# Kernel tuning notes

Hardware: AMD Instinct MI355X
Metric: run time of the kernel (lower is better)

The kernel has to match this reference:

```python
import jax, jax.numpy as jnp
from jax import lax
import numpy as np

B, L, C, PRED = 64, 512, 321, 96
PATCH, STRIDE = 16, 8
N = (L - PATCH) // STRIDE + 1 + 1  # 64 patches (after replication pad)
HID = PATCH * 2                    # expansion_factor=2
ALPHA, EPS = 0.2, 1e-5

def gelu(v):
    return jax.nn.gelu(v, approximate=False)  # torch nn.GELU default (erf)

def setup_inputs() -> dict:
    key = jax.random.key(0)
    ks = jax.random.split(key, 10)
    init = lambda k, s: (jax.random.normal(k, s) * 0.02).astype(jnp.float32)
    return dict(
        x=jax.random.normal(ks[0], (B, L, C), jnp.float32),
        rev_w=jnp.ones((C,), jnp.float32), rev_b=jnp.zeros((C,), jnp.float32),
        fc1_w=init(ks[1], (HID, PATCH)), fc1_b=jnp.zeros((HID,), jnp.float32),
        bn1_w=jnp.ones((N,), jnp.float32), bn1_b=jnp.zeros((N,), jnp.float32),
        conv_w=init(ks[2], (N, 1, 3)), conv_b=jnp.zeros((N,), jnp.float32),
        bn2_w=jnp.ones((N,), jnp.float32), bn2_b=jnp.zeros((N,), jnp.float32),
        fc2_w=init(ks[3], (PATCH, HID)), fc2_b=jnp.zeros((PATCH,), jnp.float32),
        m1_w=init(ks[4], (2 * N, N)), m1_b=jnp.zeros((2 * N,), jnp.float32),
        m2_w=init(ks[5], (N, 2 * N)), m2_b=jnp.zeros((N,), jnp.float32),
        gl_scale=jnp.full((1,), 0.1, jnp.float32),
        ln_w=jnp.ones((PATCH,), jnp.float32), ln_b=jnp.zeros((PATCH,), jnp.float32),
        seas_w=init(ks[6], (PRED, N * PATCH)), seas_b=jnp.zeros((PRED,), jnp.float32),
        tr_w=init(ks[7], (PRED, L)), tr_b=jnp.zeros((PRED,), jnp.float32),
        fus_w=init(ks[8], (PRED, 2 * PRED)), fus_b=jnp.zeros((PRED,), jnp.float32),
    )

def _batchnorm(h, w, b):
    # BatchNorm1d over channel axis N (train-mode batch stats, biased var)
    mu = h.mean((0, 2), keepdims=True)
    var = h.var((0, 2), keepdims=True)
    return (h - mu) * lax.rsqrt(var + EPS) * w[None, :, None] + b[None, :, None]

def reference(x, rev_w, rev_b, fc1_w, fc1_b, bn1_w, bn1_b, conv_w, conv_b,
              bn2_w, bn2_b, fc2_w, fc2_b, m1_w, m1_b, m2_w, m2_b, gl_scale,
              ln_w, ln_b, seas_w, seas_b, tr_w, tr_b, fus_w, fus_b):
    # --- RevIN norm (torch std is unbiased, ddof=1) ---
    mean = x.mean(1, keepdims=True)
    std = jnp.std(x, axis=1, ddof=1, keepdims=True) + EPS
    xn = (x - mean) / std * rev_w + rev_b
    # --- EMA trend/seasonal decomposition via scan ---
    xt = jnp.moveaxis(xn, 1, 0)                      # [L,B,C]
    def step(c, xi):
        t = ALPHA * xi + (1.0 - ALPHA) * c
        return t, t
    _, rest = lax.scan(step, xt[0], xt[1:])
    trend = jnp.moveaxis(jnp.concatenate([xt[:1], rest], 0), 0, 1)  # [B,L,C]
    seasonal = xn - trend
    # --- patching (replication pad right by STRIDE, unfold) ---
    s = seasonal.transpose(0, 2, 1).reshape(B * C, L)
    s = jnp.concatenate([s, jnp.broadcast_to(s[:, -1:], (B * C, STRIDE))], axis=1)
    idx = np.arange(N)[:, None] * STRIDE + np.arange(PATCH)[None, :]
    sp = s[:, idx]                                    # [B*C, N, PATCH]
    # --- IntraPatch (local): fc1 -> GELU -> BN -> depthwise conv -> GELU -> BN -> fc2 + res ---
    h = gelu(sp @ fc1_w.T + fc1_b)                    # [BC,N,HID]
    h = _batchnorm(h, bn1_w, bn1_b)
    h = lax.conv_general_dilated(h, conv_w, (1,), ((1, 1),),
                                 feature_group_count=N,
                                 dimension_numbers=('NCH', 'OIH', 'NCH'))
    h = h + conv_b[None, :, None]
    h = _batchnorm(gelu(h), bn2_w, bn2_b)
    local = h @ fc2_w.T + fc2_b + sp                  # dropout is identity (eval)
    # --- InterPatch (global): pool -> MLP -> sigmoid gate ---
    pooled = sp.mean(-1)                              # [BC,N]
    w = jax.nn.sigmoid(gelu(pooled @ m1_w.T + m1_b) @ m2_w.T + m2_b)
    glob = sp * (1.0 + gl_scale * w[..., None])
    # --- fusion 'add' + residual LayerNorm over PATCH ---
    y = sp + local + glob
    mu = y.mean(-1, keepdims=True)
    var = y.var(-1, keepdims=True)
    y = (y - mu) * lax.rsqrt(var + EPS) * ln_w + ln_b
    # --- heads ---
    s_pred = y.reshape(B * C, N * PATCH) @ seas_w.T + seas_b
    t = trend.transpose(0, 2, 1).reshape(B * C, L)
    t_pred = t @ tr_w.T + tr_b
    out = jnp.concatenate([s_pred, t_pred], -1) @ fus_w.T + fus_b
    out = out.reshape(B, C, PRED).transpose(0, 2, 1)  # [B,PRED,C]
    # --- RevIN denorm ---
    out = (out - rev_b) / rev_w
    return out * std + mean
```

## Files before the change

### kernel.cpp

```cpp
#include <hip/hip_runtime.h>
#include <hip/hip_bf16.h>
#include <math.h>

#define B_    64
#define L_    512
#define C_    321
#define PRED_ 96
#define N_    64
#define HID_  32
#define BC_   (B_*C_)
#define SROW_ 528
#define EPS_  1e-5f
#define ALPHA_ 0.2f
#define GR_   16
#define RB_   8
#define NBLK2_ (BC_/GR_)
#define NBLKH_ (BC_/8)
#define D64_  6.2771017353866808e-7f
#define STW_  548
#define UTW_  260

typedef __attribute__((ext_vector_type(8))) short bf16x8;
typedef __attribute__((ext_vector_type(4))) float f32x4;

__device__ __forceinline__ float gelu_f(float x){
  float ax = fabsf(x);
  float z  = ax * 0.70710678118654752440f;
  float t  = __builtin_amdgcn_rcpf(fmaf(0.3275911f, z, 1.0f));
  float poly = fmaf(fmaf(fmaf(fmaf(1.061405429f, t, -1.453152027f),
                   t, 1.421413741f), t, -0.284496736f), t, 0.254829592f) * t;
  float e  = __expf(-z*z);
  float erfp = fmaf(-poly, e, 1.0f);
  return fmaf(0.5f*ax, erfp, 0.5f*x);
}
__device__ __forceinline__ unsigned short bf16bits(float x){
  __hip_bfloat16 h = __float2bfloat16(x);
  return *(unsigned short*)&h;
}
__device__ __forceinline__ bf16x8 cvt8(const float* p){
  float4 a = *(const float4*)p;
  float4 b = *(const float4*)(p+4);
  bf16x8 v;
  v[0]=(short)bf16bits(a.x); v[1]=(short)bf16bits(a.y);
  v[2]=(short)bf16bits(a.z); v[3]=(short)bf16bits(a.w);
  v[4]=(short)bf16bits(b.x); v[5]=(short)bf16bits(b.y);
  v[6]=(short)bf16bits(b.z); v[7]=(short)bf16bits(b.w);
  return v;
}

__global__ __launch_bounds__(256) void k1_all(
    const float* __restrict__ x, const float* __restrict__ rev_w, const float* __restrict__ rev_b,
    const float* __restrict__ seas_w, const float* __restrict__ tr_w, const float* __restrict__ fus_w,
    const float* __restrict__ seas_b, const float* __restrict__ tr_b, const float* __restrict__ fus_b,
    float* __restrict__ s_raw, __hip_bfloat16* __restrict__ t_bf, float* __restrict__ rowpar,
    float* __restrict__ pooled,
    __hip_bfloat16* __restrict__ Wsf, __hip_bfloat16* __restrict__ Wtf,
    float* __restrict__ biasc, float* __restrict__ colsumT) {
  __shared__ float lf[8][32];
  __shared__ float psum[8][32], psq[8][32];
  __shared__ float fs[8][32];
  __shared__ float st[32*STW_];
  int tid = threadIdx.x;
  int bid = blockIdx.x;
  if (bid >= BC_/32) {
    int fb = bid - BC_/32;
    if (fb < 576) {
      int idx = fb*256 + tid;
      int j = idx / 1536, k = idx - j*1536;
      float acc = 0.f;
      if (k < 1024) {
        for (int i=0;i<96;++i) acc = fmaf(fus_w[j*192+i], seas_w[i*1024+k], acc);
        Wsf[(size_t)j*1024 + k] = __float2bfloat16(acc);
      } else {
        int l = k - 1024;
        for (int i=0;i<96;++i) acc = fmaf(fus_w[j*192+96+i], tr_w[i*512+l], acc);
        Wtf[(size_t)j*512 + l] = __float2bfloat16(acc);
      }
    } else {
      __shared__ float rowsum[96];
      if (tid < 96) {
        float s = 0.f;
        for (int l=0;l<512;++l) s += tr_w[tid*512+l];
        rowsum[tid] = s;
      }
      __syncthreads();
      if (tid < 96) {
        float acc = fus_b[tid], cs = 0.f;
        for (int i=0;i<96;++i) {
          acc = fmaf(fus_w[tid*192+i],    seas_b[i], acc);
          acc = fmaf(fus_w[tid*192+96+i], tr_b[i],   acc);
          cs  = fmaf(fus_w[tid*192+96+i], rowsum[i], cs);
        }
        biasc[tid] = acc; colsumT[tid] = cs;
      }
    }
    return;
  }
  int q = tid >> 5, r = tid & 31;
  int row0 = bid*32;
  int row = row0 + r;
  int b = row / C_, c = row - b*C_;
  const float* xp = x + (size_t)b*L_*C_ + c;
  int l0 = q*64;
  float sreg[64];
  float loc = 0.f, sum = 0.f, sq = 0.f;
  #pragma unroll
  for (int i=0;i<64;++i) {
    float v = xp[(size_t)(l0+i)*C_];
    sum += v; sq = fmaf(v,v,sq);
    loc = (q==0 && i==0) ? v : fmaf(ALPHA_, v, 0.8f*loc);
    sreg[i] = loc;
  }
  lf[q][r] = loc; psum[q][r] = sum; psq[q][r] = sq;
  __syncthreads();
  float cin = 0.f;
  for (int j=0;j<q;++j) cin = fmaf(D64_, cin, lf[j][r]);
  float S=0.f, Q=0.f;
  #pragma unroll
  for (int qq=0;qq<8;++qq){ S += psum[qq][r]; Q += psq[qq][r]; }
  float mean = S*(1.0f/512.0f);
  float var  = (Q - S*S*(1.0f/512.0f))*(1.0f/511.0f);
  var = fmaxf(var, 0.f);
  float stdv = sqrtf(var) + EPS_;
  float rwc = rev_w[c];
  float a = rwc / stdv;
  if (q==0) {
    float rbc = rev_b[c];
    float g = rbc - mean*a;
    float inva = stdv / rwc;
    ((float4*)rowpar)[row] = make_float4(a, g, mean, inva);
  }
  float prev = 0.f, f = 1.f, slast = 0.f;
  float sums8[8];
  #pragma unroll
  for (int j=0;j<8;++j) sums8[j] = 0.f;
  #pragma unroll
  for (int i=0;i<64;++i) {
    float lc = sreg[i];
    f *= 0.8f;
    float s = (q==0 && i==0) ? 0.f : fmaf(4.f, lc - prev, -f*cin);
    prev = lc;
    float sv = s * a;
    st[r*STW_ + q*64 + i] = sv;
    sums8[i>>3] += sv;
    slast = sv;
  }
  fs[q][r] = sums8[0];
  if (q==7) {
    #pragma unroll
    for (int k=0;k<8;++k) st[r*STW_ + 512 + k] = slast;
  }
  __syncthreads();
  for (int idx=tid; idx<32*130; idx+=256) {
    int rr = idx/130, g = idx - rr*130;
    float4 v = *(float4*)&st[rr*STW_ + g*4];
    *(float4*)&s_raw[(size_t)(row0+rr)*SROW_ + g*4] = v;
  }
  {
    float nf = (q < 7) ? fs[q+1][r] : 8.0f*slast;
    #pragma unroll
    for (int j=0;j<7;++j)
      pooled[(size_t)row*64 + q*8 + j] = (sums8[j] + sums8[j+1])*(1.0f/16.0f);
    pooled[(size_t)row*64 + q*8 + 7] = (sums8[7] + nf)*(1.0f/16.0f);
  }
  __syncthreads();
  unsigned* tb = (unsigned*)st;
  {
    float f2 = 1.f; unsigned lo = 0;
    #pragma unroll
    for (int i=0;i<64;++i) {
      f2 *= 0.8f;
      float tt = fmaf(f2, cin, sreg[i]) * a;
      unsigned hb = bf16bits(tt);
      if ((i&1)==0) lo = hb;
      else tb[r*UTW_ + q*32 + (i>>1)] = lo | (hb<<16);
    }
  }
  __syncthreads();
  for (int idx=tid; idx<32*64; idx+=256) {
    int rr = idx>>6, g = idx&63;
    uint4 v = *(uint4*)&tb[rr*UTW_ + g*4];
    *(uint4*)&t_bf[(size_t)(row0+rr)*512 + g*8] = v;
  }
}

__global__ __launch_bounds__(512) void k4_gate(
    const float* __restrict__ pooled,
    const float* __restrict__ m1_w, const float* __restrict__ m1_b,
    const float* __restrict__ m2_w, const float* __restrict__ m2_b,
    float* __restrict__ wl_g) {
  __shared__ __align__(16) __hip_bfloat16 buf[17408];
  int t = threadIdx.x;
  int row0 = blockIdx.x*64;
  __hip_bfloat16* A1 = buf;
  __hip_bfloat16* B1 = buf + 4608;
  __hip_bfloat16* H1 = buf;
  __hip_bfloat16* B2 = buf + 8704;
  for (int idx=t; idx<4096; idx+=512) {
    int r = idx>>6, k = idx&63;
    A1[r*72+k] = __float2bfloat16(pooled[(size_t)(row0+r)*64 + k]);
  }
  for (int idx=t; idx<8192; idx+=512) {
    int r = idx>>6, k = idx&63;
    B1[r*72+k] = __float2bfloat16(m1_w[idx]);
  }
  __syncthreads();
  int lane = t & 63, w = t >> 6;
  int fr = lane & 15, fg = lane >> 4;
  int mt = w & 3;
  int ng0 = (w>>2)*4;
  f32x4 acc1[4];
  #pragma unroll
  for (int nn=0;nn<4;++nn) acc1[nn] = (f32x4){0.f,0.f,0.f,0.f};
  #pragma unroll
  for (int ksub=0; ksub<2; ++ksub) {
    bf16x8 av = *(bf16x8*)&A1[(mt*16+fr)*72 + ksub*32 + fg*8];
    #pragma unroll
    for (int nn=0;nn<4;++nn) {
      bf16x8 bv = *(bf16x8*)&B1[((ng0+nn)*16+fr)*72 + ksub*32 + fg*8];
      acc1[nn] = __builtin_amdgcn_mfma_f32_16x16x32_bf16(av, bv, acc1[nn], 0,0,0);
    }
  }
  __syncthreads();
  #pragma unroll
  for (int nn=0;nn<4;++nn) {
    int col = (ng0+nn)*16 + fr;
    float bias = m1_b[col];
    #pragma unroll
    for (int reg=0;reg<4;++reg) {
      int row = mt*16 + fg*4 + reg;
      H1[row*136 + col] = __float2bfloat16(gelu_f(acc1[nn][reg] + bias));
    }
  }
  for (int idx=t; idx<8192; idx+=512) {
    int r = idx>>7, k = idx&127;
    B2[r*136+k] = __float2bfloat16(m2_w[idx]);
  }
  __syncthreads();
  int nt0 = (w>>2)*2;
  f32x4 acc2[2];
  #pragma unroll
  for (int nn=0;nn<2;++nn) acc2[nn] = (f32x4){0.f,0.f,0.f,0.f};
  #pragma unroll
  for (int ksub=0; ksub<4; ++ksub) {
    bf16x8 av = *(bf16x8*)&H1[(mt*16+fr)*136 + ksub*32 + fg*8];
    #pragma unroll
    for (int nn=0;nn<2;++nn) {
      bf16x8 bv = *(bf16x8*)&B2[((nt0+nn)*16+fr)*136 + ksub*32 + fg*8];
      acc2[nn] = __builtin_amdgcn_mfma_f32_16x16x32_bf16(av, bv, acc2[nn], 0,0,0);
    }
  }
  #pragma unroll
  for (int nn=0;nn<2;++nn) {
    int col = (nt0+nn)*16 + fr;
    float bias = m2_b[col];
    #pragma unroll
    for (int reg=0;reg<4;++reg) {
      int row = mt*16 + fg*4 + reg;
      wl_g[(size_t)(row0+row)*64 + col] = 1.0f/(1.0f + __expf(-(acc2[nn][reg] + bias)));
    }
  }
}

__global__ __launch_bounds__(256) void k2_bn1stats(
    const float* __restrict__ s_raw,
    const float* __restrict__ fc1_w, const float* __restrict__ fc1_b,
    float* __restrict__ partials) {
  __shared__ float sl[GR_*SROW_];
  __shared__ float red[2][GR_*64];
  int t = threadIdx.x;
  int row0 = blockIdx.x*GR_;
  for (int idx=t; idx<GR_*520; idx+=256) {
    int rr = idx/520, cc = idx - rr*520;
    sl[rr*SROW_+cc] = s_raw[(size_t)(row0+rr)*SROW_+cc];
  }
  __syncthreads();
  int lr = t >> 4, ng = t & 15;
  for (int q=0;q<4;++q) {
    int n = ng + 16*q;
    float sp[16];
    #pragma unroll
    for (int p=0;p<16;++p) sp[p] = sl[lr*SROW_ + n*8 + p];
    float s1=0.f, s2=0.f;
    #pragma unroll
    for (int hid=0; hid<32; ++hid) {
      float acc = fc1_b[hid];
      #pragma unroll
      for (int p=0;p<16;++p) acc = fmaf(sp[p], fc1_w[hid*16+p], acc);
      float gv = gelu_f(acc);
      s1 += gv; s2 = fmaf(gv,gv,s2);
    }
    red[0][lr*64+n] = s1;
    red[1][lr*64+n] = s2;
  }
  __syncthreads();
  if (t < 64) {
    float S1=0.f, S2=0.f;
    for (int lr2=0; lr2<GR_; ++lr2) { S1 += red[0][lr2*64+t]; S2 += red[1][lr2*64+t]; }
    partials[((size_t)blockIdx.x*64+t)*2+0] = S1;
    partials[((size_t)blockIdx.x*64+t)*2+1] = S2;
  }
}

__global__ __launch_bounds__(512) void k2v5_bn1_cr(
    const float* __restrict__ s_raw,
    const float* __restrict__ fc1_w, const float* __restrict__ fc1_b,
    const float* __restrict__ conv_w,
    float* __restrict__ partials, __hip_bfloat16* __restrict__ crp) {
  __shared__ __align__(16) __hip_bfloat16 Hb[4*512*8];
  __shared__ float cw[192];
  __shared__ float red[2][512];
  int t = threadIdx.x;
  int row0 = blockIdx.x*8;
  if (t < 192) cw[t] = conv_w[t];
  int lane = t & 63, w = t >> 6;
  int fr = lane & 15, fg = lane >> 4;
  bf16x8 z8 = (bf16x8){0,0,0,0,0,0,0,0};
  bf16x8 wv0 = (fg < 2) ? cvt8(&fc1_w[(0*16+fr)*16 + fg*8]) : z8;
  bf16x8 wv1 = (fg < 2) ? cvt8(&fc1_w[(1*16+fr)*16 + fg*8]) : z8;
  f32x4 acc[4][2];
  #pragma unroll
  for (int mt=0;mt<4;++mt)
    #pragma unroll
    for (int nt=0;nt<2;++nt) acc[mt][nt] = (f32x4){0.f,0.f,0.f,0.f};
  #pragma unroll
  for (int mt=0;mt<4;++mt) {
    int p = (w*4+mt)*16 + fr;
    int lr = p>>6, n = p&63;
    bf16x8 pv = (fg < 2) ? cvt8(&s_raw[(size_t)(row0+lr)*SROW_ + n*8 + fg*8]) : z8;
    acc[mt][0] = __builtin_amdgcn_mfma_f32_16x16x32_bf16(wv0, pv, acc[mt][0], 0,0,0);
    acc[mt][1] = __builtin_amdgcn_mfma_f32_16x16x32_bf16(wv1, pv, acc[mt][1], 0,0,0);
  }
  #pragma unroll
  for (int mt=0;mt<4;++mt) {
    int p = (w*4+mt)*16 + fr;
    #pragma unroll
    for (int nt=0;nt<2;++nt) {
      float4 b4 = ((const float4*)fc1_b)[nt*4+fg];
      float g0 = gelu_f(acc[mt][nt][0] + b4.x);
      float g1 = gelu_f(acc[mt][nt][1] + b4.y);
      float g2 = gelu_f(acc[mt][nt][2] + b4.z);
      float g3 = gelu_f(acc[mt][nt][3] + b4.w);
      unsigned lo = (unsigned)bf16bits(g0) | (((unsigned)bf16bits(g1))<<16);
      unsigned hi = (unsigned)bf16bits(g2) | (((unsigned)bf16bits(g3))<<16);
      int hb = nt*16 + fg*4;
      *(uint2*)&Hb[(hb>>3)*4096 + p*8 + (hb&7)] = make_uint2(lo, hi);
    }
  }
  __syncthreads();
  {
    int n = t & 63;
    uint4 u0 = *(const uint4*)&Hb[0*4096 + t*8];
    uint4 u1 = *(const uint4*)&Hb[1*4096 + t*8];
    uint4 u2 = *(const uint4*)&Hb[2*4096 + t*8];
    uint4 u3 = *(const uint4*)&Hb[3*4096 + t*8];
    unsigned uw[16] = {u0.x,u0.y,u0.z,u0.w, u1.x,u1.y,u1.z,u1.w,
                       u2.x,u2.y,u2.z,u2.w, u3.x,u3.y,u3.z,u3.w};
    float g[32];
    #pragma unroll
    for (int j=0;j<16;++j) {
      g[2*j]   = __uint_as_float(uw[j]<<16);
      g[2*j+1] = __uint_as_float(uw[j] & 0xffff0000u);
    }
    float s1=0.f, s2=0.f;
    #pragma unroll
    for (int k=0;k<32;++k) { s1 += g[k]; s2 = fmaf(g[k], g[k], s2); }
    float w0=cw[n*3], wm=cw[n*3+1], wp=cw[n*3+2];
    unsigned wds[16]; unsigned crlo = 0;
    float prevv = 0.f;
    #pragma unroll
    for (int k=0;k<32;++k) {
      float cr = fmaf(prevv, w0, fmaf(g[k], wm, (k<31) ? g[k+1]*wp : 0.f));
      prevv = g[k];
      unsigned hbits = bf16bits(cr);
      if ((k&1)==0) crlo = hbits; else wds[k>>1] = crlo | (hbits<<16);
    }
    uint4* dst = (uint4*)&crp[((size_t)row0*64 + t)*32];
    dst[0] = make_uint4(wds[0],wds[1],wds[2],wds[3]);
    dst[1] = make_uint4(wds[4],wds[5],wds[6],wds[7]);
    dst[2] = make_uint4(wds[8],wds[9],wds[10],wds[11]);
    dst[3] = make_uint4(wds[12],wds[13],wds[14],wds[15]);
    red[0][t] = s1;
    red[1][t] = s2;
  }
  __syncthreads();
  if (t < 64) {
    float S1=0.f, S2=0.f;
    #pragma unroll
    for (int lr2=0; lr2<8; ++lr2) { S1 += red[0][lr2*64+t]; S2 += red[1][lr2*64+t]; }
    partials[((size_t)blockIdx.x*64+t)*2+0] = S1;
    partials[((size_t)blockIdx.x*64+t)*2+1] = S2;
  }
}

__global__ __launch_bounds__(256) void k_bnreduce(
    const float* __restrict__ partials, int nblk,
    const float* __restrict__ bnw, const float* __restrict__ bnb,
    float* __restrict__ scale, float* __restrict__ shift) {
  __shared__ float red[2][256];
  int n = blockIdx.x, t = threadIdx.x;
  float s1=0.f, s2=0.f;
  for (int i=t; i<nblk; i+=256) {
    s1 += partials[((size_t)i*64+n)*2+0];
    s2 += partials[((size_t)i*64+n)*2+1];
  }
  red[0][t]=s1; red[1][t]=s2;
  __syncthreads();
  for (int off=128; off>0; off>>=1) {
    if (t<off) { red[0][t]+=red[0][t+off]; red[1][t]+=red[1][t+off]; }
    __syncthreads();
  }
  if (t==0) {
    const float count = (float)BC_ * 32.0f;
    float mu = red[0][0]/count;
    float var = red[1][0]/count - mu*mu;
    float sc = rsqrtf(var + EPS_) * bnw[n];
    scale[n] = sc;
    shift[n] = bnb[n] - mu*sc;
  }
}

__global__ __launch_bounds__(256) void k3_bn2stats(
    const float* __restrict__ s_raw,
    const float* __restrict__ fc1_w, const float* __restrict__ fc1_b,
    const float* __restrict__ scale1, const float* __restrict__ shift1,
    const float* __restrict__ conv_w, const float* __restrict__ conv_b,
    float* __restrict__ partials) {
  __shared__ float sl[GR_*SROW_];
  __shared__ float sc1[64], sh1[64], cw[192], cb[64];
  __shared__ float red[2][GR_*64];
  int t = threadIdx.x;
  int row0 = blockIdx.x*GR_;
  if (t < 64) { sc1[t]=scale1[t]; sh1[t]=shift1[t]; cb[t]=conv_b[t]; }
  if (t >= 64 && t < 256) cw[t-64] = conv_w[t-64];
  __syncthreads();
  for (int idx=t; idx<GR_*520; idx+=256) {
    int rr = idx/520, cc = idx - rr*520;
    sl[rr*SROW_+cc] = s_raw[(size_t)(row0+rr)*SROW_+cc];
  }
  __syncthreads();
  int lr = t >> 4, ng = t & 15;
  for (int q=0;q<4;++q) {
    int n = ng + 16*q;
    float sp[16];
    #pragma unroll
    for (int p=0;p<16;++p) sp[p] = sl[lr*SROW_ + n*8 + p];
    float scn = sc1[n], shn = sh1[n];
    float h[32];
    #pragma unroll
    for (int hid=0; hid<32; ++hid) {
      float acc = fc1_b[hid];
      #pragma unroll
      for (int p=0;p<16;++p) acc = fmaf(sp[p], fc1_w[hid*16+p], acc);
      h[hid] = fmaf(gelu_f(acc), scn, shn);
    }
    float w0=cw[n*3], wm=cw[n*3+1], wpp=cw[n*3+2], cbn=cb[n];
    float s1=0.f, s2=0.f, prev=0.f;
    #pragma unroll
    for (int k2=0;k2<32;++k2) {
      float cur = h[k2];
      float cv = cbn;
      cv = fmaf(prev, w0, cv);
      cv = fmaf(cur, wm, cv);
      if (k2<31) cv = fmaf(h[k2+1], wpp, cv);
      float gv = gelu_f(cv);
      s1 += gv; s2 = fmaf(gv,gv,s2);
      prev = cur;
    }
    red[0][lr*64+n]=s1; red[1][lr*64+n]=s2;
  }
  __syncthreads();
  if (t < 64) {
    float S1=0.f, S2=0.f;
    for (int lr2=0; lr2<GR_; ++lr2) { S1 += red[0][lr2*64+t]; S2 += red[1][lr2*64+t]; }
    partials[((size_t)blockIdx.x*64+t)*2+0] = S1;
    partials[((size_t)blockIdx.x*64+t)*2+1] = S2;
  }
}

__global__ __launch_bounds__(512) void k3v2_bn2stats(
    __hip_bfloat16* __restrict__ crp,
    const float* __restrict__ scale1, const float* __restrict__ shift1,
    const float* __restrict__ conv_w, const float* __restrict__ conv_b,
    float* __restrict__ partials) {
  __shared__ float sc1[64], sh0l[64], shml[64], sh31l[64];
  __shared__ float red[2][512];
  int t = threadIdx.x;
  int row0 = blockIdx.x*8;
  if (t < 64) {
    float w0=conv_w[t*3], wm=conv_w[t*3+1], wp=conv_w[t*3+2];
    float s1v=shift1[t], cbv=conv_b[t];
    sc1[t]  = scale1[t];
    sh0l[t] = fmaf(s1v, wm+wp, cbv);
    shml[t] = fmaf(s1v, w0+wm+wp, cbv);
    sh31l[t]= fmaf(s1v, w0+wm, cbv);
  }
  __syncthreads();
  int lr = t>>6, n = t&63;
  uint4* crb = (uint4*)&crp[((size_t)(row0+lr)*64 + n)*32];
  uint4 u0=crb[0], u1=crb[1], u2=crb[2], u3=crb[3];
  unsigned uw[16] = {u0.x,u0.y,u0.z,u0.w, u1.x,u1.y,u1.z,u1.w,
                     u2.x,u2.y,u2.z,u2.w, u3.x,u3.y,u3.z,u3.w};
  float sc1n = sc1[n];
  float shm = shml[n];
  float s1=0.f, s2=0.f;
  unsigned wds[16];
  #pragma unroll
  for (int j=0;j<16;++j) {
    unsigned u = uw[j];
    float c0 = __uint_as_float(u<<16);
    float c1 = __uint_as_float(u & 0xffff0000u);
    float sh_0 = (j==0)  ? sh0l[n]  : shm;
    float sh_1 = (j==15) ? sh31l[n] : shm;
    float g0 = gelu_f(fmaf(c0, sc1n, sh_0));
    float g1 = gelu_f(fmaf(c1, sc1n, sh_1));
    s1 += g0 + g1;
    s2 = fmaf(g0,g0, fmaf(g1,g1, s2));
    wds[j] = (unsigned)bf16bits(g0) | (((unsigned)bf16bits(g1))<<16);
  }
  crb[0] = make_uint4(wds[0],wds[1],wds[2],wds[3]);
  crb[1] = make_uint4(wds[4],wds[5],wds[6],wds[7]);
  crb[2] = make_uint4(wds[8],wds[9],wds[10],wds[11]);
  crb[3] = make_uint4(wds[12],wds[13],wds[14],wds[15]);
  red[0][t]=s1; red[1][t]=s2;
  __syncthreads();
  if (t < 64) {
    float S1=0.f, S2=0.f;
    #pragma unroll
    for (int lr2=0; lr2<8; ++lr2) { S1 += red[0][lr2*64+t]; S2 += red[1][lr2*64+t]; }
    partials[((size_t)blockIdx.x*64+t)*2+0] = S1;
    partials[((size_t)blockIdx.x*64+t)*2+1] = S2;
  }
}

__global__ __launch_bounds__(256) void k5a_pipeline(
    const float* __restrict__ s_raw, const float* __restrict__ wl_g,
    const float* __restrict__ fc1_w, const float* __restrict__ fc1_b,
    const float* __restrict__ scale1, const float* __restrict__ shift1,
    const float* __restrict__ conv_w, const float* __restrict__ conv_b,
    const float* __restrict__ scale2, const float* __restrict__ shift2,
    const float* __restrict__ fc2_w, const float* __restrict__ fc2_b,
    const float* __restrict__ gl_scale,
    const float* __restrict__ ln_w, const float* __restrict__ ln_b,
    __hip_bfloat16* __restrict__ ybf) {
  __shared__ float sl[RB_*SROW_];
  __shared__ float cw[192], cb[64];
  __shared__ float sc1[64], sh1[64], sc2[64], sh2[64];
  int t = threadIdx.x;
  int row0 = blockIdx.x*RB_;
  if (t<64) { sc1[t]=scale1[t]; sh1[t]=shift1[t]; sc2[t]=scale2[t]; sh2[t]=shift2[t]; cb[t]=conv_b[t]; }
  if (t>=64 && t<256) cw[t-64]=conv_w[t-64];
  __syncthreads();
  for (int idx=t; idx<RB_*520; idx+=256) {
    int rr = idx/520, cc = idx - rr*520;
    sl[rr*SROW_+cc] = s_raw[(size_t)(row0+rr)*SROW_+cc];
  }
  __syncthreads();
  float glv = gl_scale[0];
  for (int idx=t; idx<RB_*64; idx+=256) {
    int rr = idx>>6, n = idx&63;
    float wlv = wl_g[(size_t)row0*64 + idx];
    float h[32];
    {
      float sp[16];
      #pragma unroll
      for (int p=0;p<16;++p) sp[p] = sl[rr*SROW_ + n*8 + p];
      float scn=sc1[n], shn=sh1[n];
      #pragma unroll
      for (int hid=0;hid<32;++hid) {
        float acc=fc1_b[hid];
        #pragma unroll
        for (int p=0;p<16;++p) acc=fmaf(sp[p], fc1_w[hid*16+p], acc);
        h[hid]=fmaf(gelu_f(acc), scn, shn);
      }
    }
    {
      float w0=cw[n*3], wm=cw[n*3+1], wpp=cw[n*3+2], cbn=cb[n];
      float sc2n=sc2[n], sh2n=sh2[n];
      float prev=0.f;
      #pragma unroll
      for (int k2=0;k2<32;++k2) {
        float cur = h[k2];
        float cv = cbn;
        cv = fmaf(prev, w0, cv);
        cv = fmaf(cur, wm, cv);
        if (k2<31) cv = fmaf(h[k2+1], wpp, cv);
        h[k2] = fmaf(gelu_f(cv), sc2n, sh2n);
        prev = cur;
      }
    }
    float yv[16];
    #pragma unroll
    for (int p=0;p<16;++p) {
      float acc=fc2_b[p];
      #pragma unroll
      for (int hid=0;hid<32;++hid) acc=fmaf(h[hid], fc2_w[p*32+hid], acc);
      yv[p]=acc;
    }
    float smul = 3.0f + glv*wlv;
    float mu=0.f;
    #pragma unroll
    for (int p=0;p<16;++p) {
      yv[p]=fmaf(sl[rr*SROW_ + n*8 + p], smul, yv[p]);
      mu+=yv[p];
    }
    mu *= (1.0f/16.0f);
    float var=0.f;
    #pragma unroll
    for (int p=0;p<16;++p){ float d=yv[p]-mu; var=fmaf(d,d,var); }
    var *= (1.0f/16.0f);
    float rs = rsqrtf(var + EPS_);
    unsigned int wds[8];
    #pragma unroll
    for (int j=0;j<8;++j) {
      unsigned int lo = bf16bits(fmaf((yv[2*j]-mu)*rs,   ln_w[2*j],   ln_b[2*j]));
      unsigned int hi = bf16bits(fmaf((yv[2*j+1]-mu)*rs, ln_w[2*j+1], ln_b[2*j+1]));
      wds[j] = lo | (hi<<16);
    }
    size_t ybase = (size_t)(row0+rr)*1024 + n*16;
    uint4* dst = (uint4*)&ybf[ybase];
    dst[0] = make_uint4(wds[0],wds[1],wds[2],wds[3]);
    dst[1] = make_uint4(wds[4],wds[5],wds[6],wds[7]);
  }
}

__global__ __launch_bounds__(512) void k5a_v3(
    const float* __restrict__ s_raw, const float* __restrict__ wl_g,
    const __hip_bfloat16* __restrict__ g2p,
    const float* __restrict__ scale2, const float* __restrict__ shift2,
    const float* __restrict__ fc2_w, const float* __restrict__ fc2_b,
    const float* __restrict__ gl_scale,
    const float* __restrict__ ln_w, const float* __restrict__ ln_b,
    __hip_bfloat16* __restrict__ ybf) {
  __shared__ float sc2[64], sh2[64];
  int t = threadIdx.x;
  int row0 = blockIdx.x*RB_;
  if (t < 64) { sc2[t]=scale2[t]; sh2[t]=shift2[t]; }
  __syncthreads();
  int rr = t>>6, n = t&63;
  int row = row0 + rr;
  float glv = gl_scale[0];
  float wlv = wl_g[(size_t)row*64 + n];
  const uint4* crb = (const uint4*)&g2p[((size_t)row*64 + n)*32];
  uint4 u0=crb[0], u1=crb[1], u2=crb[2], u3=crb[3];
  unsigned uw[16] = {u0.x,u0.y,u0.z,u0.w, u1.x,u1.y,u1.z,u1.w,
                     u2.x,u2.y,u2.z,u2.w, u3.x,u3.y,u3.z,u3.w};
  float sc2n = sc2[n], sh2n = sh2[n];
  float yv[16];
  #pragma unroll
  for (int p=0;p<16;++p) yv[p] = fc2_b[p];
  #pragma unroll
  for (int j=0;j<16;++j) {
    unsigned u = uw[j];
    int k0 = 2*j, k1 = 2*j+1;
    float g0 = __uint_as_float(u<<16);
    float g1 = __uint_as_float(u & 0xffff0000u);
    float h2a = fmaf(g0, sc2n, sh2n);
    float h2b = fmaf(g1, sc2n, sh2n);
    #pragma unroll
    for (int p=0;p<16;++p)
      yv[p] = fmaf(h2a, fc2_w[p*32+k0], fmaf(h2b, fc2_w[p*32+k1], yv[p]));
  }
  const float* sp_g = &s_raw[(size_t)row*SROW_ + n*8];
  float4 s0 = *(const float4*)(sp_g);
  float4 s1v = *(const float4*)(sp_g+4);
  float4 s2v = *(const float4*)(sp_g+8);
  float4 s3 = *(const float4*)(sp_g+12);
  float sp[16] = {s0.x,s0.y,s0.z,s0.w, s1v.x,s1v.y,s1v.z,s1v.w,
                  s2v.x,s2v.y,s2v.z,s2v.w, s3.x,s3.y,s3.z,s3.w};
  float smul = 3.0f + glv*wlv;
  float mu=0.f;
  #pragma unroll
  for (int p=0;p<16;++p) {
    yv[p] = fmaf(sp[p], smul, yv[p]);
    mu += yv[p];
  }
  mu *= (1.0f/16.0f);
  float var=0.f;
  #pragma unroll
  for (int p=0;p<16;++p){ float d=yv[p]-mu; var=fmaf(d,d,var); }
  var *= (1.0f/16.0f);
  float rs = rsqrtf(var + EPS_);
  unsigned int wds[8];
  #pragma unroll
  for (int j=0;j<8;++j) {
    unsigned int lo = bf16bits(fmaf((yv[2*j]-mu)*rs,   ln_w[2*j],   ln_b[2*j]));
    unsigned int hi = bf16bits(fmaf((yv[2*j+1]-mu)*rs, ln_w[2*j+1], ln_b[2*j+1]));
    wds[j] = lo | (hi<<16);
  }
  size_t ybase = (size_t)row*1024 + n*16;
  uint4* dst = (uint4*)&ybf[ybase];
  dst[0] = make_uint4(wds[0],wds[1],wds[2],wds[3]);
  dst[1] = make_uint4(wds[4],wds[5],wds[6],wds[7]);
}

__global__ __launch_bounds__(384) void k5b_gemm(
    const __hip_bfloat16* __restrict__ ybf, const __hip_bfloat16* __restrict__ tbf,
    const __hip_bfloat16* __restrict__ Wsf, const __hip_bfloat16* __restrict__ Wtf,
    const float* __restrict__ rowpar, const float* __restrict__ rev_b,
    const float* __restrict__ biasc, const float* __restrict__ colsumT,
    float* __restrict__ out) {
  __shared__ __align__(16) __hip_bfloat16 As[2*16*72];
  __shared__ __align__(16) __hip_bfloat16 Bs[2*96*72];
  __shared__ float rp[64];
  __shared__ float rbl[16];
  __shared__ int   obase[16];
  __shared__ float bcl[96], csl[96];
  int tid = threadIdx.x;
  int row0 = blockIdx.x*16;
  if (tid < 64) rp[tid] = rowpar[(size_t)row0*4 + tid];
  if (tid >= 64 && tid < 80) {
    int lr = tid-64;
    int row = row0 + lr; int b = row/C_; int c = row - b*C_;
    rbl[lr] = rev_b[c]; obase[lr] = b*PRED_*C_ + c;
  }
  if (tid >= 96 && tid < 192) { bcl[tid-96]=biasc[tid-96]; csl[tid-96]=colsumT[tid-96]; }
  int lane = tid & 63, w = tid >> 6;
  int fr = lane & 15, fg = lane >> 4;
  bool a0 = tid < 128;
  int r0 = a0 ? (tid>>3) : ((tid-128)>>3);
  int c0 = a0 ? (tid&7)  : ((tid-128)&7);
  int r1 = (tid+256)>>3, c1 = (tid+256)&7;
  bool h2 = tid < 128;
  int r2 = (tid+640)>>3, c2 = (tid+640)&7;
  f32x4 acc = (f32x4){0.f,0.f,0.f,0.f};

  uint4 v0, v1, v2;
  auto LOAD = [&](int ks){
    const __hip_bfloat16* Ag; const __hip_bfloat16* Bg; int K; int kofs;
    if (ks < 8) { Ag = tbf + (size_t)row0*512;  Bg = Wtf; K = 512;  kofs = ks*64; }
    else        { Ag = ybf + (size_t)row0*1024; Bg = Wsf; K = 1024; kofs = (ks-8)*64; }
    v0 = a0 ? *(const uint4*)(Ag + (size_t)r0*K + kofs + c0*8)
            : *(const uint4*)(Bg + (size_t)r0*K + kofs + c0*8);
    v1 = *(const uint4*)(Bg + (size_t)r1*K + kofs + c1*8);
    if (h2) v2 = *(const uint4*)(Bg + (size_t)r2*K + kofs + c2*8);
  };

  LOAD(0);
  int cur = 0;
  for (int ks=0; ks<24; ++ks) {
    __hip_bfloat16* Ab = &As[cur*16*72];
    __hip_bfloat16* Bb = &Bs[cur*96*72];
    if (a0) *(uint4*)&Ab[r0*72 + c0*8] = v0;
    else    *(uint4*)&Bb[r0*72 + c0*8] = v0;
    *(uint4*)&Bb[r1*72 + c1*8] = v1;
    if (h2) *(uint4*)&Bb[r2*72 + c2*8] = v2;
    __syncthreads();
    if (ks < 23) LOAD(ks+1);
    #pragma unroll
    for (int ksub=0; ksub<2; ++ksub) {
      bf16x8 av = *(bf16x8*)&Ab[fr*72 + ksub*32 + fg*8];
      bf16x8 bv = *(bf16x8*)&Bb[(w*16+fr)*72 + ksub*32 + fg*8];
      acc = __builtin_amdgcn_mfma_f32_16x16x32_bf16(av, bv, acc, 0,0,0);
    }
    cur ^= 1;
  }
  {
    int col = w*16 + fr;
    float cs = csl[col], bc = bcl[col];
    #pragma unroll
    for (int reg=0;reg<4;++reg) {
      int rloc = fg*4 + reg;
      float g = rp[rloc*4+1], meanv = rp[rloc*4+2], inva = rp[rloc*4+3];
      float val = acc[reg] + g*cs + bc;
      val = (val - rbl[rloc])*inva + meanv;
      out[(size_t)obase[rloc] + (size_t)col*C_] = val;
    }
  }
}

extern "C" void kernel_launch(void* const* d_in, const int* in_sizes, int n_in,
                              void* d_out, int out_size, void* d_ws, size_t ws_size,
                              hipStream_t stream) {
  const float* x      = (const float*)d_in[0];
  const float* rev_w  = (const float*)d_in[1];
  const float* rev_b  = (const float*)d_in[2];
  const float* fc1_w  = (const float*)d_in[3];
  const float* fc1_b  = (const float*)d_in[4];
  const float* bn1_w  = (const float*)d_in[5];
  const float* bn1_b  = (const float*)d_in[6];
  const float* conv_w = (const float*)d_in[7];
  const float* conv_b = (const float*)d_in[8];
  const float* bn2_w  = (const float*)d_in[9];
  const float* bn2_b  = (const float*)d_in[10];
  const float* fc2_w  = (const float*)d_in[11];
  const float* fc2_b  = (const float*)d_in[12];
  const float* m1_w   = (const float*)d_in[13];
  const float* m1_b   = (const float*)d_in[14];
  const float* m2_w   = (const float*)d_in[15];
  const float* m2_b   = (const float*)d_in[16];
  const float* gl     = (const float*)d_in[17];
  const float* ln_w   = (const float*)d_in[18];
  const float* ln_b   = (const float*)d_in[19];
  const float* seas_w = (const float*)d_in[20];
  const float* seas_b = (const float*)d_in[21];
  const float* tr_w   = (const float*)d_in[22];
  const float* tr_b   = (const float*)d_in[23];
  const float* fus_w  = (const float*)d_in[24];
  const float* fus_b  = (const float*)d_in[25];
  float* out = (float*)d_out;
  float* ws = (float*)d_ws;

  __hip_bfloat16* Wsf  = (__hip_bfloat16*)(ws);
  __hip_bfloat16* Wtf  = (__hip_bfloat16*)(ws + 49152);
  float* biasc   = ws + 73728;
  float* colsumT = ws + 73856;
  float* scale1  = ws + 73984;
  float* shift1  = ws + 74048;
  float* scale2  = ws + 74112;
  float* shift2  = ws + 74176;
  float* partials= ws + 74240;
  float* rowpar  = ws + 238592;
  float* s_raw   = ws + 320768;
  __hip_bfloat16* t_bf = (__hip_bfloat16*)(ws + 11168000);
  __hip_bfloat16* ybf  = (__hip_bfloat16*)(ws + 16427264);
  float* pooled  = ws + 26945792;
  float* wl_g    = ws + 28260608;
  __hip_bfloat16* crp  = (__hip_bfloat16*)(ws + 29575424);
  float* pbig    = ws + 16427264;
  const size_t NEED = (29575424ull + 21037056ull) * 4ull;
  bool big = (ws_size >= NEED);

  hipLaunchKernelGGL(k1_all, dim3(BC_/32 + 577), dim3(256), 0, stream,
    x, rev_w, rev_b, seas_w, tr_w, fus_w, seas_b, tr_b, fus_b,
    s_raw, t_bf, rowpar, pooled, Wsf, Wtf, biasc, colsumT);
  hipLaunchKernelGGL(k4_gate, dim3(BC_/64), dim3(512), 0, stream, pooled, m1_w, m1_b, m2_w, m2_b, wl_g);
  if (big) {
    hipLaunchKernelGGL(k2v5_bn1_cr, dim3(NBLKH_), dim3(512), 0, stream, s_raw, fc1_w, fc1_b, conv_w, pbig, crp);
    hipLaunchKernelGGL(k_bnreduce, dim3(64), dim3(256), 0, stream, pbig, NBLKH_, bn1_w, bn1_b, scale1, shift1);
    hipLaunchKernelGGL(k3v2_bn2stats, dim3(NBLKH_), dim3(512), 0, stream, crp, scale1, shift1, conv_w, conv_b, pbig);
    hipLaunchKernelGGL(k_bnreduce, dim3(64), dim3(256), 0, stream, pbig, NBLKH_, bn2_w, bn2_b, scale2, shift2);
    hipLaunchKernelGGL(k5a_v3, dim3(NBLKH_), dim3(512), 0, stream,
      s_raw, wl_g, crp, scale2, shift2, fc2_w, fc2_b, gl, ln_w, ln_b, ybf);
  } else {
    hipLaunchKernelGGL(k2_bn1stats, dim3(NBLK2_), dim3(256), 0, stream, s_raw, fc1_w, fc1_b, partials);
    hipLaunchKernelGGL(k_bnreduce, dim3(64), dim3(256), 0, stream, partials, NBLK2_, bn1_w, bn1_b, scale1, shift1);
    hipLaunchKernelGGL(k3_bn2stats, dim3(NBLK2_), dim3(256), 0, stream, s_raw, fc1_w, fc1_b, scale1, shift1, conv_w, conv_b, partials);
    hipLaunchKernelGGL(k_bnreduce, dim3(64), dim3(256), 0, stream, partials, NBLK2_, bn2_w, bn2_b, scale2, shift2);
    hipLaunchKernelGGL(k5a_pipeline, dim3(BC_/RB_), dim3(256), 0, stream,
      s_raw, wl_g, fc1_w, fc1_b, scale1, shift1, conv_w, conv_b,
      scale2, shift2, fc2_w, fc2_b, gl, ln_w, ln_b, ybf);
  }
  hipLaunchKernelGGL(k5b_gemm, dim3(BC_/16), dim3(384), 0, stream,
    ybf, t_bf, Wsf, Wtf, rowpar, rev_b, biasc, colsumT, out);
}
```

Before: 218.6 us.

## Apply fc2 before BN2 affine so GELU pass emits compact fp16 projections

BN2 is an affine map per channel, so fc2(BN2(g)) is rewritten as scale2*(fc2 g) + shift2*rowsum(fc2_w) + fc2_b. The BN2 statistics kernel now also computes the 16-wide fc2 projection of the GELU outputs and stores it as fp16 into the ybf buffer. It no longer writes the 32-wide bf16 GELU activations back. The final pre-head kernel reads this smaller tensor and overwrites it in place with the LayerNorm output, cutting memory traffic and the per-element 32x16 matmul there. The cost is extra FMA work in the stats kernel, fp16 rounding of the projections, and reuse of workspace regions such as ybf and the pooled buffer.

```diff
diff --git a/kernel.cpp b/kernel.cpp
--- a/kernel.cpp
+++ b/kernel.cpp
@@ -1,5 +1,6 @@
 #include <hip/hip_runtime.h>
 #include <hip/hip_bf16.h>
+#include <hip/hip_fp16.h>
 #include <math.h>
 
 #define B_    64
@@ -37,6 +38,14 @@
   __hip_bfloat16 h = __float2bfloat16(x);
   return *(unsigned short*)&h;
 }
+__device__ __forceinline__ unsigned short f16bits(float x){
+  __half h = __float2half(x);
+  return *(unsigned short*)&h;
+}
+__device__ __forceinline__ float f16val(unsigned short u){
+  __half h = *(__half*)&u;
+  return __half2float(h);
+}
 __device__ __forceinline__ bf16x8 cvt8(const float* p){
   float4 a = *(const float4*)p;
   float4 b = *(const float4*)(p+4);
@@ -52,10 +61,11 @@
     const float* __restrict__ x, const float* __restrict__ rev_w, const float* __restrict__ rev_b,
     const float* __restrict__ seas_w, const float* __restrict__ tr_w, const float* __restrict__ fus_w,
     const float* __restrict__ seas_b, const float* __restrict__ tr_b, const float* __restrict__ fus_b,
+    const float* __restrict__ fc2_w,
     float* __restrict__ s_raw, __hip_bfloat16* __restrict__ t_bf, float* __restrict__ rowpar,
     float* __restrict__ pooled,
     __hip_bfloat16* __restrict__ Wsf, __hip_bfloat16* __restrict__ Wtf,
-    float* __restrict__ biasc, float* __restrict__ colsumT) {
+    float* __restrict__ biasc, float* __restrict__ colsumT, float* __restrict__ Wsum) {
   __shared__ float lf[8][32];
   __shared__ float psum[8][32], psq[8][32];
   __shared__ float fs[8][32];
@@ -78,6 +88,13 @@
       }
     } else {
       __shared__ float rowsum[96];
+      if (tid >= 96 && tid < 112) {
+        int j = tid - 96;
+        float s = 0.f;
+        #pragma unroll
+        for (int k=0;k<32;++k) s += fc2_w[j*32+k];
+        Wsum[j] = s;
+      }
       if (tid < 96) {
         float s = 0.f;
         for (int l=0;l<512;++l) s += tr_w[tid*512+l];
@@ -478,11 +495,12 @@
   }
 }
 
-__global__ __launch_bounds__(512) void k3v2_bn2stats(
-    __hip_bfloat16* __restrict__ crp,
+__global__ __launch_bounds__(512) void k3v3_bn2_u(
+    const __hip_bfloat16* __restrict__ crp,
     const float* __restrict__ scale1, const float* __restrict__ shift1,
     const float* __restrict__ conv_w, const float* __restrict__ conv_b,
-    float* __restrict__ partials) {
+    const float* __restrict__ fc2_w,
+    float* __restrict__ partials, __half* __restrict__ Ub) {
   __shared__ float sc1[64], sh0l[64], shml[64], sh31l[64];
   __shared__ float red[2][512];
   int t = threadIdx.x;
@@ -496,15 +514,15 @@
     sh31l[t]= fmaf(s1v, w0+wm, cbv);
   }
   __syncthreads();
-  int lr = t>>6, n = t&63;
-  uint4* crb = (uint4*)&crp[((size_t)(row0+lr)*64 + n)*32];
+  int n = t&63;
+  const uint4* crb = (const uint4*)&crp[((size_t)row0*64 + t)*32];
   uint4 u0=crb[0], u1=crb[1], u2=crb[2], u3=crb[3];
   unsigned uw[16] = {u0.x,u0.y,u0.z,u0.w, u1.x,u1.y,u1.z,u1.w,
                      u2.x,u2.y,u2.z,u2.w, u3.x,u3.y,u3.z,u3.w};
   float sc1n = sc1[n];
   float shm = shml[n];
+  float g[32];
   float s1=0.f, s2=0.f;
-  unsigned wds[16];
   #pragma unroll
   for (int j=0;j<16;++j) {
     unsigned u = uw[j];
@@ -514,14 +532,25 @@
     float sh_1 = (j==15) ? sh31l[n] : shm;
     float g0 = gelu_f(fmaf(c0, sc1n, sh_0));
     float g1 = gelu_f(fmaf(c1, sc1n, sh_1));
+    g[2*j]   = g0;
+    g[2*j+1] = g1;
     s1 += g0 + g1;
     s2 = fmaf(g0,g0, fmaf(g1,g1, s2));
-    wds[j] = (unsigned)bf16bits(g0) | (((unsigned)bf16bits(g1))<<16);
-  }
-  crb[0] = make_uint4(wds[0],wds[1],wds[2],wds[3]);
-  crb[1] = make_uint4(wds[4],wds[5],wds[6],wds[7]);
-  crb[2] = make_uint4(wds[8],wds[9],wds[10],wds[11]);
-  crb[3] = make_uint4(wds[12],wds[13],wds[14],wds[15]);
+  }
+  unsigned wds[8];
+  #pragma unroll
+  for (int jj=0;jj<8;++jj) {
+    float ua = 0.f, ub = 0.f;
+    #pragma unroll
+    for (int k=0;k<32;++k) {
+      ua = fmaf(fc2_w[(2*jj  )*32+k], g[k], ua);
+      ub = fmaf(fc2_w[(2*jj+1)*32+k], g[k], ub);
+    }
+    wds[jj] = (unsigned)f16bits(ua) | (((unsigned)f16bits(ub))<<16);
+  }
+  uint4* dst = (uint4*)&Ub[((size_t)row0*64 + t)*16];
+  dst[0] = make_uint4(wds[0],wds[1],wds[2],wds[3]);
+  dst[1] = make_uint4(wds[4],wds[5],wds[6],wds[7]);
   red[0][t]=s1; red[1][t]=s2;
   __syncthreads();
   if (t < 64) {
@@ -624,42 +653,34 @@
   }
 }
 
-__global__ __launch_bounds__(512) void k5a_v3(
+__global__ __launch_bounds__(512) void k5a_v4(
     const float* __restrict__ s_raw, const float* __restrict__ wl_g,
-    const __hip_bfloat16* __restrict__ g2p,
     const float* __restrict__ scale2, const float* __restrict__ shift2,
-    const float* __restrict__ fc2_w, const float* __restrict__ fc2_b,
+    const float* __restrict__ Wsum, const float* __restrict__ fc2_b,
     const float* __restrict__ gl_scale,
     const float* __restrict__ ln_w, const float* __restrict__ ln_b,
     __hip_bfloat16* __restrict__ ybf) {
-  __shared__ float sc2[64], sh2[64];
+  __shared__ float sc2l[64], sh2l[64];
   int t = threadIdx.x;
   int row0 = blockIdx.x*RB_;
-  if (t < 64) { sc2[t]=scale2[t]; sh2[t]=shift2[t]; }
+  if (t < 64) { sc2l[t]=scale2[t]; sh2l[t]=shift2[t]; }
   __syncthreads();
   int rr = t>>6, n = t&63;
   int row = row0 + rr;
   float glv = gl_scale[0];
   float wlv = wl_g[(size_t)row*64 + n];
-  const uint4* crb = (const uint4*)&g2p[((size_t)row*64 + n)*32];
-  uint4 u0=crb[0], u1=crb[1], u2=crb[2], u3=crb[3];
-  unsigned uw[16] = {u0.x,u0.y,u0.z,u0.w, u1.x,u1.y,u1.z,u1.w,
-                     u2.x,u2.y,u2.z,u2.w, u3.x,u3.y,u3.z,u3.w};
-  float sc2n = sc2[n], sh2n = sh2[n];
+  size_t pbase = ((size_t)row*64 + n)*16;
+  uint4* uptr = (uint4*)&ybf[pbase];
+  uint4 a = uptr[0], b = uptr[1];
+  unsigned hw[8] = {a.x,a.y,a.z,a.w, b.x,b.y,b.z,b.w};
+  float sc2n = sc2l[n], sh2n = sh2l[n];
   float yv[16];
   #pragma unroll
-  for (int p=0;p<16;++p) yv[p] = fc2_b[p];
-  #pragma unroll
-  for (int j=0;j<16;++j) {
-    unsigned u = uw[j];
-    int k0 = 2*j, k1 = 2*j+1;
-    float g0 = __uint_as_float(u<<16);
-    float g1 = __uint_as_float(u & 0xffff0000u);
-    float h2a = fmaf(g0, sc2n, sh2n);
-    float h2b = fmaf(g1, sc2n, sh2n);
-    #pragma unroll
-    for (int p=0;p<16;++p)
-      yv[p] = fmaf(h2a, fc2_w[p*32+k0], fmaf(h2b, fc2_w[p*32+k1], yv[p]));
+  for (int j=0;j<8;++j) {
+    float U0 = f16val((unsigned short)(hw[j] & 0xffffu));
+    float U1 = f16val((unsigned short)(hw[j] >> 16));
+    yv[2*j]   = fmaf(sc2n, U0, fmaf(sh2n, Wsum[2*j],   fc2_b[2*j]));
+    yv[2*j+1] = fmaf(sc2n, U1, fmaf(sh2n, Wsum[2*j+1], fc2_b[2*j+1]));
   }
   const float* sp_g = &s_raw[(size_t)row*SROW_ + n*8];
   float4 s0 = *(const float4*)(sp_g);
@@ -688,10 +709,8 @@
     unsigned int hi = bf16bits(fmaf((yv[2*j+1]-mu)*rs, ln_w[2*j+1], ln_b[2*j+1]));
     wds[j] = lo | (hi<<16);
   }
-  size_t ybase = (size_t)row*1024 + n*16;
-  uint4* dst = (uint4*)&ybf[ybase];
-  dst[0] = make_uint4(wds[0],wds[1],wds[2],wds[3]);
-  dst[1] = make_uint4(wds[4],wds[5],wds[6],wds[7]);
+  uptr[0] = make_uint4(wds[0],wds[1],wds[2],wds[3]);
+  uptr[1] = make_uint4(wds[4],wds[5],wds[6],wds[7]);
 }
 
 __global__ __launch_bounds__(384) void k5b_gemm(
@@ -810,6 +829,7 @@
   float* scale2  = ws + 74112;
   float* shift2  = ws + 74176;
   float* partials= ws + 74240;
+  float* Wsum    = ws + 74240;
   float* rowpar  = ws + 238592;
   float* s_raw   = ws + 320768;
   __hip_bfloat16* t_bf = (__hip_bfloat16*)(ws + 11168000);
@@ -817,21 +837,22 @@
   float* pooled  = ws + 26945792;
   float* wl_g    = ws + 28260608;
   __hip_bfloat16* crp  = (__hip_bfloat16*)(ws + 29575424);
-  float* pbig    = ws + 16427264;
+  float* ppool   = ws + 26945792;
+  __half* Uh     = (__half*)ybf;
   const size_t NEED = (29575424ull + 21037056ull) * 4ull;
   bool big = (ws_size >= NEED);
 
   hipLaunchKernelGGL(k1_all, dim3(BC_/32 + 577), dim3(256), 0, stream,
-    x, rev_w, rev_b, seas_w, tr_w, fus_w, seas_b, tr_b, fus_b,
-    s_raw, t_bf, rowpar, pooled, Wsf, Wtf, biasc, colsumT);
+    x, rev_w, rev_b, seas_w, tr_w, fus_w, seas_b, tr_b, fus_b, fc2_w,
+    s_raw, t_bf, rowpar, pooled, Wsf, Wtf, biasc, colsumT, Wsum);
   hipLaunchKernelGGL(k4_gate, dim3(BC_/64), dim3(512), 0, stream, pooled, m1_w, m1_b, m2_w, m2_b, wl_g);
   if (big) {
-    hipLaunchKernelGGL(k2v5_bn1_cr, dim3(NBLKH_), dim3(512), 0, stream, s_raw, fc1_w, fc1_b, conv_w, pbig, crp);
-    hipLaunchKernelGGL(k_bnreduce, dim3(64), dim3(256), 0, stream, pbig, NBLKH_, bn1_w, bn1_b, scale1, shift1);
-    hipLaunchKernelGGL(k3v2_bn2stats, dim3(NBLKH_), dim3(512), 0, stream, crp, scale1, shift1, conv_w, conv_b, pbig);
-    hipLaunchKernelGGL(k_bnreduce, dim3(64), dim3(256), 0, stream, pbig, NBLKH_, bn2_w, bn2_b, scale2, shift2);
-    hipLaunchKernelGGL(k5a_v3, dim3(NBLKH_), dim3(512), 0, stream,
-      s_raw, wl_g, crp, scale2, shift2, fc2_w, fc2_b, gl, ln_w, ln_b, ybf);
+    hipLaunchKernelGGL(k2v5_bn1_cr, dim3(NBLKH_), dim3(512), 0, stream, s_raw, fc1_w, fc1_b, conv_w, ppool, crp);
+    hipLaunchKernelGGL(k_bnreduce, dim3(64), dim3(256), 0, stream, ppool, NBLKH_, bn1_w, bn1_b, scale1, shift1);
+    hipLaunchKernelGGL(k3v3_bn2_u, dim3(NBLKH_), dim3(512), 0, stream, crp, scale1, shift1, conv_w, conv_b, fc2_w, ppool, Uh);
+    hipLaunchKernelGGL(k_bnreduce, dim3(64), dim3(256), 0, stream, ppool, NBLKH_, bn2_w, bn2_b, scale2, shift2);
+    hipLaunchKernelGGL(k5a_v4, dim3(NBLKH_), dim3(512), 0, stream,
+      s_raw, wl_g, scale2, shift2, Wsum, fc2_b, gl, ln_w, ln_b, ybf);
   } else {
     hipLaunchKernelGGL(k2_bn1stats, dim3(NBLK2_), dim3(256), 0, stream, s_raw, fc1_w, fc1_b, partials);
     hipLaunchKernelGGL(k_bnreduce, dim3(64), dim3(256), 0, stream, partials, NBLK2_, bn1_w, bn1_b, scale1, shift1);
```

New measurement: 206.9 us, median of 2. 1.06x faster.
